# Kernel tuning notes

Hardware: AMD Instinct MI355X
Metric: run time of the kernel (lower is better)

## Reference

```python
import jax, jax.numpy as jnp
import numpy as np

NB_LABELS = 8        # number of distinct node labels
NB_EDGE_LABELS = 4   # number of distinct edge (bond) labels
N = 32               # order of every graph (card_max, all graphs padded/equal)
SINKHORN_ITERS = 10  # svd.eps_assign2(..., 10)


def costs_from_weighs(node_weighs, edge_weighs):
    cn = jax.nn.relu(node_weighs)
    ce = jax.nn.relu(edge_weighs)
    iu = jnp.triu_indices(NB_LABELS, k=1)
    node_costs = jnp.zeros((NB_LABELS, NB_LABELS), dtype=cn.dtype).at[iu].set(cn[:-1])
    node_costs = node_costs + node_costs.T
    iu2 = jnp.triu_indices(NB_EDGE_LABELS, k=1)
    edge_costs = jnp.zeros((NB_EDGE_LABELS, NB_EDGE_LABELS), dtype=ce.dtype).at[iu2].set(ce[:-1])
    edge_costs = edge_costs + edge_costs.T
    return node_costs, cn[-1], edge_costs, ce[-1]


def sinkhorn(S, iters):
    # eps-assignment: alternate row/col normalization, last row/col scale fixed to 1
    for _ in range(iters):
        r = 1.0 / S.sum(axis=1)
        r = r.at[-1].set(1.0)
        S = S * r[:, None]
        c = 1.0 / S.sum(axis=0)
        c = c.at[-1].set(1.0)
        S = S * c[None, :]
    return S


def pair_ged(A1, A2, l1, l2, node_costs, nodeInsDel, edge_costs, edgeInsDel):
    # A1, A2: (N+1, N+1) int padded labeled adjacency; l1, l2: (N,) int node labels
    n1 = N + 1
    b1 = A1 != 0
    b2 = A2 != 0
    # edge insertion/deletion indicator: (not e1 and e2) or (e1 and not e2)
    ins_del = jnp.logical_or(
        jnp.einsum('ij,kl->ijkl', ~b1, b2),
        jnp.einsum('ij,kl->ijkl', b1, ~b2)).astype(jnp.float32)
    # edge substitution: sum_{p!=q} edge_costs[p,q] * [A1==p+1] * [A2==q+1]
    lab_ids = jnp.arange(1, NB_EDGE_LABELS + 1)
    E1 = (A1[None] == lab_ids[:, None, None]).astype(jnp.float32)  # (L, n1, n1)
    E2 = (A2[None] == lab_ids[:, None, None]).astype(jnp.float32)
    subst = jnp.einsum('pij,qkl,pq->ijkl', E1, E2, edge_costs)  # diag(edge_costs)=0
    C4 = edgeInsDel * ins_del + subst
    # torch cat/unbind reshuffle: C[(j,k),(i,l)] = C4[i,j,k,l]
    C = jnp.transpose(C4, (1, 2, 0, 3)).reshape(n1 * n1, n1 * n1)
    # diagonal vector D: node subst for (i<N, j<N), nodeInsDel on last row/col, 0 at corner
    Dmat = jnp.full((n1, n1), nodeInsDel, dtype=jnp.float32)
    Dmat = Dmat.at[:N, :N].set(node_costs[l1][:, l2])
    Dmat = Dmat.at[N, N].set(0.0)
    c_diag = Dmat.reshape(-1)                       # diag(C) after masking
    Doff = C * (1.0 - jnp.eye(n1 * n1, dtype=C.dtype))  # C with diagonal zeroed
    # mapping_from_cost returns x0 = sinkhorn(exp(-0.5*c), 10)
    v = sinkhorn(jnp.exp(-0.5 * Dmat), SINKHORN_ITERS).reshape(-1)
    return 0.5 * (v @ (Doff @ v)) + c_diag @ v


def setup_inputs() -> dict:
    key = jax.random.key(0)
    k1, k2, k3, k4, k5 = jax.random.split(key, 5)
    G, P = 64, 64
    nw = 0.01 * (1.0 + 0.1 * jax.random.uniform(k1, (NB_LABELS * (NB_LABELS - 1) // 2 + 1,)))
    nw = nw.at[-1].set(0.03)
    ew = 0.01 * (1.0 + 0.1 * jax.random.uniform(k2, (NB_EDGE_LABELS * (NB_EDGE_LABELS - 1) // 2 + 1,)))
    ew = ew.at[-1].set(0.02)
    R = jax.random.randint(k3, (G, N, N), 0, NB_EDGE_LABELS + 1)
    Au = jnp.triu(R, 1)
    A = (Au + jnp.transpose(Au, (0, 2, 1))).astype(jnp.int32)  # symmetric labeled adjacency
    labels = jax.random.randint(k4, (G, N), 0, NB_LABELS, dtype=jnp.int32)
    pairs = jax.random.randint(k5, (P, 2), 0, G, dtype=jnp.int32)
    return {"node_weighs": nw.astype(jnp.float32), "edge_weighs": ew.astype(jnp.float32),
            "A": A, "labels": labels, "pairs": pairs}


def reference(node_weighs, edge_weighs, A, labels, pairs):
    node_costs, nodeInsDel, edge_costs, edgeInsDel = costs_from_weighs(node_weighs, edge_weighs)
    A1 = jnp.pad(A[pairs[:, 0]], ((0, 0), (0, 1), (0, 1)))  # (P, N+1, N+1)
    A2 = jnp.pad(A[pairs[:, 1]], ((0, 0), (0, 1), (0, 1)))
    l1 = labels[pairs[:, 0]]
    l2 = labels[pairs[:, 1]]
    ged = jax.vmap(pair_ged, in_axes=(0, 0, 0, 0, None, None, None, None))(
        A1, A2, l1, l2, node_costs, nodeInsDel, edge_costs, edgeInsDel)
    return (ged - ged.min()) / (ged.max() - ged.min())
```

## Files before the change

### kernel.cpp

```cpp
#include <hip/hip_runtime.h>
#include <math.h>
#include <stdint.h>

constexpr int NQ    = 33;
constexpr int NQP   = 34;
constexpr int HP    = 36;
constexpr int NSQ   = NQ * NQ;
constexpr int NL    = 8;
constexpr int NEL   = 4;
constexpr int NN    = 32;
constexpr int ITERS = 10;
constexpr int BLK   = 1024;
constexpr unsigned int MAGIC = 0x5A5A5A5Au;

__global__ __launch_bounds__(BLK, 1) void ged_fused(
    const float* __restrict__ nw, const float* __restrict__ ew,
    const int* __restrict__ A, const int* __restrict__ labels,
    const int* __restrict__ pairs, float* __restrict__ ged_ws,
    unsigned int* __restrict__ tag, float* __restrict__ out, int P)
{
    __shared__ __align__(16) float S[NQ][NQP];
    __shared__ __align__(16) float S0T[NQ][NQP];
    __shared__ __align__(16) float H[5][NQ][HP];
    __shared__ unsigned char A1s[NQ][36];
    __shared__ unsigned char A2s[NQ][36];
    __shared__ float ncost[NL][NL];
    __shared__ float encost[NL][NL];
    __shared__ float ec[NEL][NEL];
    __shared__ __align__(16) float rr[NQ], cc[NQ], rsum[NQ];
    __shared__ float sNID, sEID, sENID;
    __shared__ int l1s[NN], l2s[NN];
    __shared__ float wredq[16], wredl[16];

    const int t  = threadIdx.x;
    const int p  = blockIdx.x;
    const int g1 = pairs[2*p+0], g2 = pairs[2*p+1];

    if (t < 28) {
        int i = (t>=27)?6 : (t>=25)?5 : (t>=22)?4 : (t>=18)?3 : (t>=13)?2 : (t>=7)?1 : 0;
        int off = (i==0)?0 : (i==1)?7 : (i==2)?13 : (i==3)?18 : (i==4)?22 : (i==5)?25 : 27;
        int j = t - off + i + 1;
        float v = fmaxf(nw[t], 0.f);
        ncost[i][j] = v; ncost[j][i] = v;
        float e = __expf(-0.5f * v);
        encost[i][j] = e; encost[j][i] = e;
    } else if (t == 28) {
        float v = fmaxf(nw[28], 0.f);
        sNID = v; sENID = __expf(-0.5f * v);
    } else if (t >= 32 && t < 38) {
        int q = t - 32;
        int ei = (q<3)?0 : (q<5)?1 : 2;
        int ej = (q<3)?q+1 : (q<5)?q-1 : 3;
        float v = fmaxf(ew[q], 0.f);
        ec[ei][ej] = v; ec[ej][ei] = v;
    } else if (t == 38) {
        sEID = fmaxf(ew[6], 0.f);
    } else if (t >= 40 && t < 48) {
        int q = t - 40;
        ncost[q][q] = 0.f; encost[q][q] = 1.f;
    } else if (t >= 48 && t < 52) {
        int q = t - 48;
        ec[q][q] = 0.f;
    }
    if (t >= 64  && t < 64 + NN)  l1s[t - 64]  = labels[g1*NN + (t - 64)];
    if (t >= 96  && t < 96 + NN)  l2s[t - 96]  = labels[g2*NN + (t - 96)];
    for (int c0 = t; c0 < NSQ; c0 += BLK) {
        int i = c0 / NQ, j = c0 - i*NQ;
        int a1 = (i < NN && j < NN) ? A[g1*NN*NN + i*NN + j] : 0;
        int a2 = (i < NN && j < NN) ? A[g2*NN*NN + i*NN + j] : 0;
        A1s[i][j] = (unsigned char)a1;
        A2s[i][j] = (unsigned char)a2;
    }
    __syncthreads();

    const float NID = sNID, EID = sEID, ENID = sENID;
    const float e01 = ec[0][1], e02 = ec[0][2], e03 = ec[0][3];
    const float e12 = ec[1][2], e13 = ec[1][3], e23 = ec[2][3];

    for (int c0 = t; c0 < NSQ; c0 += BLK) {
        int i = c0 / NQ, j = c0 - i*NQ;
        float e = (i < NN && j < NN) ? encost[l1s[i]][l2s[j]]
                                     : ((i == NN && j == NN) ? 1.f : ENID);
        S[i][j]   = e;
        S0T[j][i] = e;
    }
    __syncthreads();

    if (t < 64) {
        const int half = t >> 5;
        const int id   = t & 31;
        float sreg[17], treg[17];
        int   idxr[17];
        #pragma unroll
        for (int m = 0; m < 17; ++m) {
            int hs = 17 + m;
            int src = half ? ((hs <= 31) ? hs : 63) : m;
            idxr[m] = src << 2;
        }
        #pragma unroll
        for (int m = 0; m < 17; ++m) {
            int j = half ? (17 + m) : m;
            float sv = (half && m == 16) ? 0.f : S[id][j];
            float tv = (half && m == 16) ? 0.f : S0T[id][j];
            sreg[m] = sv; treg[m] = tv;
        }

        float cval = 1.0f, rval = 1.0f;
        for (int it = 0; it < ITERS; ++it) {
            float a0=0.f, a1=0.f, a2=0.f, a3=0.f;
            #pragma unroll
            for (int m = 0; m < 17; ++m) {
                float cm = __int_as_float(
                    __builtin_amdgcn_ds_bpermute(idxr[m], __float_as_int(cval)));
                if ((m & 3) == 0) a0 += sreg[m]*cm;
                else if ((m & 3) == 1) a1 += sreg[m]*cm;
                else if ((m & 3) == 2) a2 += sreg[m]*cm;
                else a3 += sreg[m]*cm;
            }
            float part = (a0+a1)+(a2+a3);
            part += __shfl_xor(part, 32);
            rval = __builtin_amdgcn_rcpf(part);
            if (t == 63) rval = 1.0f;
            float b0=0.f, b1=0.f, b2=0.f, b3=0.f;
            #pragma unroll
            for (int m = 0; m < 17; ++m) {
                float rm = __int_as_float(
                    __builtin_amdgcn_ds_bpermute(idxr[m], __float_as_int(rval)));
                if ((m & 3) == 0) b0 += treg[m]*rm;
                else if ((m & 3) == 1) b1 += treg[m]*rm;
                else if ((m & 3) == 2) b2 += treg[m]*rm;
                else b3 += treg[m]*rm;
            }
            float part2 = (b0+b1)+(b2+b3);
            part2 += __shfl_xor(part2, 32);
            cval = __builtin_amdgcn_rcpf(part2);
            if (t == 63) cval = 1.0f;
        }

        float a0=0.f, a1=0.f, a2=0.f, a3=0.f;
        #pragma unroll
        for (int m = 0; m < 17; ++m) {
            float cm = __int_as_float(
                __builtin_amdgcn_ds_bpermute(idxr[m], __float_as_int(cval)));
            if ((m & 3) == 0) a0 += sreg[m]*cm;
            else if ((m & 3) == 1) a1 += sreg[m]*cm;
            else if ((m & 3) == 2) a2 += sreg[m]*cm;
            else a3 += sreg[m]*cm;
        }
        float part = (a0+a1)+(a2+a3);
        part += __shfl_xor(part, 32);
        if (!half) { rr[id] = rval; cc[id] = cval; rsum[id] = rval * part; }

        float csum = cval;
        csum += __shfl_xor(csum, 16);
        csum += __shfl_xor(csum, 8);
        csum += __shfl_xor(csum, 4);
        csum += __shfl_xor(csum, 2);
        csum += __shfl_xor(csum, 1);
        if (t == 0) {
            rr[32] = 1.f; cc[32] = 1.f;
            rsum[32] = ENID * csum + 1.0f;
        }
    }
    __syncthreads();

    for (int c0 = t; c0 < NSQ; c0 += BLK) {
        int i = c0 / NQ, j = c0 - i*NQ;
        S[i][j] *= rr[i] * cc[j];
    }
    __syncthreads();

    for (int c0 = t; c0 < NSQ; c0 += BLK) {
        int i = c0 / NQ, k = c0 - i*NQ;
        const float* Si = &S[i][0];
        const uint32_t* Aw = (const uint32_t*)&A2s[k][0];
        float p1=0.f, p2=0.f, p3=0.f, p4=0.f;
        #pragma unroll
        for (int l = 0; l < NQ; ++l) {
            float v = Si[l];
            int a2v = (int)((Aw[l >> 2] >> ((l & 3) * 8)) & 255u);
            p1 += (a2v == 1) ? v : 0.f;
            p2 += (a2v == 2) ? v : 0.f;
            p3 += (a2v == 3) ? v : 0.f;
            p4 += (a2v == 4) ? v : 0.f;
        }
        float t4 = (p1 + p2) + (p3 + p4);
        float p0 = rsum[i] - t4;
        H[0][i][k] = EID * t4;
        H[1][i][k] = EID * p0 +            e01*p2 + e02*p3 + e03*p4;
        H[2][i][k] = EID * p0 + e01*p1 +            e12*p3 + e13*p4;
        H[3][i][k] = EID * p0 + e02*p1 + e12*p2 +            e23*p4;
        H[4][i][k] = EID * p0 + e03*p1 + e13*p2 + e23*p3;
    }
    __syncthreads();

    float qpart = 0.f, lpart = 0.f;
    if (t < 363) {
        const int j  = t / 11;
        const int ig = t - j*11;
        float Vr[34];
        const float2* Sj2 = (const float2*)&S[j][0];
        #pragma unroll
        for (int m = 0; m < 17; ++m) {
            float2 w = Sj2[m];
            Vr[2*m] = w.x; Vr[2*m+1] = w.y;
        }
        #pragma unroll
        for (int ii = 0; ii < 3; ++ii) {
            const int i = ig*3 + ii;
            const int x = A1s[i][j];
            const float* Hx = &H[x][i][0];
            float d0=0.f, d1=0.f, d2=0.f, d3=0.f;
            #pragma unroll
            for (int k = 0; k < 32; k += 4) {
                d0 += Vr[k+0]*Hx[k+0]; d1 += Vr[k+1]*Hx[k+1];
                d2 += Vr[k+2]*Hx[k+2]; d3 += Vr[k+3]*Hx[k+3];
            }
            qpart += ((d0+d1)+(d2+d3)) + Vr[32]*Hx[32];
            float d;
            if (i < NN && j < NN) d = ncost[l1s[i]][l2s[j]];
            else                  d = (i == NN && j == NN) ? 0.f : NID;
            lpart += d * S[i][j];
        }
    }

    #pragma unroll
    for (int off = 32; off > 0; off >>= 1) {
        qpart += __shfl_down(qpart, off);
        lpart += __shfl_down(lpart, off);
    }
    if ((t & 63) == 0) { wredq[t>>6] = qpart; wredl[t>>6] = lpart; }
    __syncthreads();
    if (t < 16) {
        float q = wredq[t], l = wredl[t];
        q += __shfl_down(q, 8); l += __shfl_down(l, 8);
        q += __shfl_down(q, 4); l += __shfl_down(l, 4);
        q += __shfl_down(q, 2); l += __shfl_down(l, 2);
        q += __shfl_down(q, 1); l += __shfl_down(l, 1);
        if (t == 0) {
            unsigned int bits = __float_as_uint(0.5f * q + l);
            __hip_atomic_store((unsigned int*)&ged_ws[p], bits,
                               __ATOMIC_RELAXED, __HIP_MEMORY_SCOPE_AGENT);
            __hip_atomic_store(&tag[p], bits ^ MAGIC,
                               __ATOMIC_RELEASE, __HIP_MEMORY_SCOPE_AGENT);
        }
    }

    if (p == 0 && t < 64) {
        unsigned int tv, wv;
        do {
            tv = __hip_atomic_load(&tag[t], __ATOMIC_ACQUIRE,
                                   __HIP_MEMORY_SCOPE_AGENT);
            wv = __hip_atomic_load((unsigned int*)&ged_ws[t], __ATOMIC_ACQUIRE,
                                   __HIP_MEMORY_SCOPE_AGENT);
        } while ((tv ^ MAGIC) != wv);
        float g = __uint_as_float(wv);
        float mn = g, mx = g;
        #pragma unroll
        for (int off = 32; off > 0; off >>= 1) {
            mn = fminf(mn, __shfl_xor(mn, off));
            mx = fmaxf(mx, __shfl_xor(mx, off));
        }
        out[t] = (g - mn) / (mx - mn);
    }
}

extern "C" void kernel_launch(void* const* d_in, const int* in_sizes, int n_in,
                              void* d_out, int out_size, void* d_ws, size_t ws_size,
                              hipStream_t stream) {
    const float* nw     = (const float*)d_in[0];
    const float* ew     = (const float*)d_in[1];
    const int*   A      = (const int*)d_in[2];
    const int*   labels = (const int*)d_in[3];
    const int*   pairs  = (const int*)d_in[4];
    const int P = in_sizes[4] / 2;

    float*        ged_ws = (float*)d_ws;
    unsigned int* tag    = (unsigned int*)((char*)d_ws + 4096);

    ged_fused<<<P, BLK, 0, stream>>>(nw, ew, A, labels, pairs, ged_ws, tag,
                                     (float*)d_out, P);
}
```

Baseline: 20.57 us.

## Split each pair across four blocks by row slabs for final contraction

Launches four blocks per graph pair, and each block computes the H tensor and the quadratic/linear terms for only its slab of rows (8 or 9 of 33). Each block still redoes the full setup and Sinkhorn iterations, and writes its partial result to a per-slot tagged workspace. Block 0 spins on all four slots per pair and sums them before min/max normalization. This spreads the contraction over more CUs at the cost of redundant Sinkhorn work and four times as many blocks that block 0 must wait on.

```diff
diff --git a/kernel.cpp b/kernel.cpp
--- a/kernel.cpp
+++ b/kernel.cpp
@@ -16,8 +16,8 @@
 __global__ __launch_bounds__(BLK, 1) void ged_fused(
     const float* __restrict__ nw, const float* __restrict__ ew,
     const int* __restrict__ A, const int* __restrict__ labels,
-    const int* __restrict__ pairs, float* __restrict__ ged_ws,
-    unsigned int* __restrict__ tag, float* __restrict__ out, int P)
+    const int* __restrict__ pairs, float* __restrict__ slot_val,
+    unsigned int* __restrict__ slot_tag, float* __restrict__ out, int P)
 {
     __shared__ __align__(16) float S[NQ][NQP];
     __shared__ __align__(16) float S0T[NQ][NQP];
@@ -33,7 +33,11 @@
     __shared__ float wredq[16], wredl[16];
 
     const int t  = threadIdx.x;
-    const int p  = blockIdx.x;
+    const int p  = blockIdx.x >> 2;
+    const int s  = blockIdx.x & 3;
+    const int r0 = 8 * s;
+    const int nr = (s == 3) ? 9 : 8;
+    const int cells = nr * NQ;
     const int g1 = pairs[2*p+0], g2 = pairs[2*p+1];
 
     if (t < 28) {
@@ -170,8 +174,8 @@
     }
     __syncthreads();
 
-    for (int c0 = t; c0 < NSQ; c0 += BLK) {
-        int i = c0 / NQ, k = c0 - i*NQ;
+    if (t < cells) {
+        int i = r0 + t / NQ, k = t - (t / NQ) * NQ;
         const float* Si = &S[i][0];
         const uint32_t* Aw = (const uint32_t*)&A2s[k][0];
         float p1=0.f, p2=0.f, p3=0.f, p4=0.f;
@@ -195,33 +199,23 @@
     __syncthreads();
 
     float qpart = 0.f, lpart = 0.f;
-    if (t < 363) {
-        const int j  = t / 11;
-        const int ig = t - j*11;
-        float Vr[34];
-        const float2* Sj2 = (const float2*)&S[j][0];
-        #pragma unroll
-        for (int m = 0; m < 17; ++m) {
-            float2 w = Sj2[m];
-            Vr[2*m] = w.x; Vr[2*m+1] = w.y;
-        }
-        #pragma unroll
-        for (int ii = 0; ii < 3; ++ii) {
-            const int i = ig*3 + ii;
-            const int x = A1s[i][j];
-            const float* Hx = &H[x][i][0];
-            float d0=0.f, d1=0.f, d2=0.f, d3=0.f;
-            #pragma unroll
-            for (int k = 0; k < 32; k += 4) {
-                d0 += Vr[k+0]*Hx[k+0]; d1 += Vr[k+1]*Hx[k+1];
-                d2 += Vr[k+2]*Hx[k+2]; d3 += Vr[k+3]*Hx[k+3];
-            }
-            qpart += ((d0+d1)+(d2+d3)) + Vr[32]*Hx[32];
-            float d;
-            if (i < NN && j < NN) d = ncost[l1s[i]][l2s[j]];
-            else                  d = (i == NN && j == NN) ? 0.f : NID;
-            lpart += d * S[i][j];
-        }
+    if (t < cells) {
+        const int i = r0 + t / NQ;
+        const int j = t - (t / NQ) * NQ;
+        const int x = A1s[i][j];
+        const float* Hx = &H[x][i][0];
+        const float* Sj = &S[j][0];
+        float d0=0.f, d1=0.f, d2=0.f, d3=0.f;
+        #pragma unroll
+        for (int k = 0; k < 32; k += 4) {
+            d0 += Sj[k+0]*Hx[k+0]; d1 += Sj[k+1]*Hx[k+1];
+            d2 += Sj[k+2]*Hx[k+2]; d3 += Sj[k+3]*Hx[k+3];
+        }
+        qpart = ((d0+d1)+(d2+d3)) + Sj[32]*Hx[32];
+        float d;
+        if (i < NN && j < NN) d = ncost[l1s[i]][l2s[j]];
+        else                  d = (i == NN && j == NN) ? 0.f : NID;
+        lpart = d * S[i][j];
     }
 
     #pragma unroll
@@ -238,23 +232,29 @@
         q += __shfl_down(q, 2); l += __shfl_down(l, 2);
         q += __shfl_down(q, 1); l += __shfl_down(l, 1);
         if (t == 0) {
+            const int m = (p << 2) | s;
             unsigned int bits = __float_as_uint(0.5f * q + l);
-            __hip_atomic_store((unsigned int*)&ged_ws[p], bits,
+            __hip_atomic_store((unsigned int*)&slot_val[m], bits,
                                __ATOMIC_RELAXED, __HIP_MEMORY_SCOPE_AGENT);
-            __hip_atomic_store(&tag[p], bits ^ MAGIC,
+            __hip_atomic_store(&slot_tag[m], bits ^ MAGIC,
                                __ATOMIC_RELEASE, __HIP_MEMORY_SCOPE_AGENT);
         }
     }
 
-    if (p == 0 && t < 64) {
-        unsigned int tv, wv;
-        do {
-            tv = __hip_atomic_load(&tag[t], __ATOMIC_ACQUIRE,
-                                   __HIP_MEMORY_SCOPE_AGENT);
-            wv = __hip_atomic_load((unsigned int*)&ged_ws[t], __ATOMIC_ACQUIRE,
-                                   __HIP_MEMORY_SCOPE_AGENT);
-        } while ((tv ^ MAGIC) != wv);
-        float g = __uint_as_float(wv);
+    if (blockIdx.x == 0 && t < 64) {
+        float g = 0.f;
+        #pragma unroll
+        for (int ss = 0; ss < 4; ++ss) {
+            const int m = (t << 2) | ss;
+            unsigned int tv, wv;
+            do {
+                tv = __hip_atomic_load(&slot_tag[m], __ATOMIC_ACQUIRE,
+                                       __HIP_MEMORY_SCOPE_AGENT);
+                wv = __hip_atomic_load((unsigned int*)&slot_val[m], __ATOMIC_ACQUIRE,
+                                       __HIP_MEMORY_SCOPE_AGENT);
+            } while ((tv ^ MAGIC) != wv);
+            g += __uint_as_float(wv);
+        }
         float mn = g, mx = g;
         #pragma unroll
         for (int off = 32; off > 0; off >>= 1) {
@@ -275,9 +275,9 @@
     const int*   pairs  = (const int*)d_in[4];
     const int P = in_sizes[4] / 2;
 
-    float*        ged_ws = (float*)d_ws;
-    unsigned int* tag    = (unsigned int*)((char*)d_ws + 4096);
-
-    ged_fused<<<P, BLK, 0, stream>>>(nw, ew, A, labels, pairs, ged_ws, tag,
-                                     (float*)d_out, P);
+    float*        slot_val = (float*)d_ws;
+    unsigned int* slot_tag = (unsigned int*)((char*)d_ws + 8192);
+
+    ged_fused<<<4 * P, BLK, 0, stream>>>(nw, ew, A, labels, pairs,
+                                         slot_val, slot_tag, (float*)d_out, P);
 }
```

After: 18.03 us. 12.3% less time.
